# Optimization experiments

Hardware: AMD Instinct MI355X
Metric: run time of the kernel (lower is better)

Reference implementation:

```python
import jax, jax.numpy as jnp
import numpy as np

D_MODEL = 512


def _xavier(key, shape, gain=1.0):
    fan_in, fan_out = shape[1], shape[0]
    a = gain * np.sqrt(6.0 / (fan_in + fan_out))
    return jax.random.uniform(key, shape, jnp.float32, -a, a)


def setup_inputs() -> dict:
    key = jax.random.key(0)
    kx, kq, kk, kv, ko = jax.random.split(key, 5)
    x = jax.random.normal(kx, (16, D_MODEL, 32, 32), jnp.float32)
    Wq = _xavier(kq, (D_MODEL, D_MODEL))
    Wk = _xavier(kk, (D_MODEL, D_MODEL))
    Wv = _xavier(kv, (D_MODEL, D_MODEL))
    Wo = _xavier(ko, (D_MODEL, D_MODEL), gain=1e-05)
    bq = jnp.zeros((D_MODEL,), jnp.float32)
    bk = jnp.zeros((D_MODEL,), jnp.float32)
    bv = jnp.zeros((D_MODEL,), jnp.float32)
    bo = jnp.zeros((D_MODEL,), jnp.float32)
    return {"x": x, "Wq": Wq, "bq": bq, "Wk": Wk, "bk": bk, "Wv": Wv, "bv": bv, "Wo": Wo, "bo": bo}


def _proj_tokens(x, W, b):
    # 1x1 conv == channel matmul, then flatten spatial to tokens: [B, H*W, C]
    B, C, H, Wd = x.shape
    y = jnp.einsum('bchw,oc->bhwo', x, W) + b  # [B, H, W, C_out]
    return y.reshape(B, H * Wd, -1)


def reference(x, Wq, bq, Wk, bk, Wv, bv, Wo, bo):
    B, C, H, W = x.shape
    temperature = jnp.asarray(C, x.dtype) ** 0.5
    q = _proj_tokens(x, Wq, bq)  # [B, N, C]
    k = _proj_tokens(x, Wk, bk)
    v = _proj_tokens(x, Wv, bv)
    scores = jnp.einsum('bnc,bmc->bnm', q / temperature, k)  # [B, N, N]
    attention = jax.nn.softmax(scores, axis=-1)
    out = jnp.einsum('bnm,bmc->bnc', attention, v)  # [B, N, C]
    out = out.reshape(B, H, W, C)
    out = jnp.einsum('bhwc,oc->bohw', out, Wo) + bo[None, :, None, None]
    return (x + out, attention)
```

## Files before the change

### kernel.cpp

```cpp
#include <hip/hip_runtime.h>
#include <hip/hip_bf16.h>

#define DM 512
#define NTOK 1024
#define NB 16

typedef _Float16 f16;
typedef _Float16 half8 __attribute__((ext_vector_type(8)));
typedef _Float16 half4_t __attribute__((ext_vector_type(4)));
typedef float f32x4 __attribute__((ext_vector_type(4)));

__device__ __forceinline__ void gload16(const void* g, void* l) {
    __builtin_amdgcn_global_load_lds(
        (const __attribute__((address_space(1))) void*)g,
        (__attribute__((address_space(3))) void*)l, 16, 0, 0);
}

__global__ __launch_bounds__(256)
void transpose_x_kernel(const float* __restrict__ x, f16* __restrict__ xt) {
    __shared__ float tile[32][33];
    int b = blockIdx.z;
    int n0 = blockIdx.x * 32, c0 = blockIdx.y * 32;
    int tx = threadIdx.x, ty = threadIdx.y;
    const float* xb = x + (size_t)b * DM * NTOK + (size_t)(c0 + ty) * NTOK + n0 + tx * 4;
    float4 v = *(const float4*)xb;
    tile[ty][tx * 4 + 0] = v.x; tile[ty][tx * 4 + 1] = v.y;
    tile[ty][tx * 4 + 2] = v.z; tile[ty][tx * 4 + 3] = v.w;
    __syncthreads();
    half4_t h = {(f16)tile[tx * 4 + 0][ty], (f16)tile[tx * 4 + 1][ty],
                 (f16)tile[tx * 4 + 2][ty], (f16)tile[tx * 4 + 3][ty]};
    *(half4_t*)&xt[(size_t)b * NTOK * DM + (size_t)(n0 + ty) * DM + c0 + tx * 4] = h;
}

__global__ __launch_bounds__(256)
void convert_wqkv_kernel(const float* __restrict__ Wq, const float* __restrict__ Wk,
                         const float* __restrict__ Wv, const float* __restrict__ bq,
                         const float* __restrict__ bk, const float* __restrict__ bv,
                         f16* __restrict__ dst, float* __restrict__ bdst,
                         float* __restrict__ rowsum) {
    int i = blockIdx.x * 256 + threadIdx.x;
    int row = i >> 9, col = i & 511;
    float v = (row < 512) ? Wq[i] : (row < 1024) ? Wk[(row - 512) * 512 + col]
                                                 : Wv[(row - 1024) * 512 + col];
    dst[i] = (f16)v;
    if (i < 1536)
        bdst[i] = (i < 512) ? bq[i] : (i < 1024) ? bk[i - 512] : bv[i - 1024];
    if (blockIdx.x < 64) rowsum[blockIdx.x * 256 + threadIdx.x] = 0.f;
}

__global__ __launch_bounds__(256)
void convert_w_kernel(const float* __restrict__ src, f16* __restrict__ dst, int n) {
    int i = blockIdx.x * 256 + threadIdx.x;
    if (i < n) dst[i] = (f16)src[i];
}

__global__ __launch_bounds__(256)
void transpose_v_kernel(const f16* __restrict__ vtok, f16* __restrict__ vh) {
    __shared__ f16 tile[32][36];
    int b = blockIdx.z;
    int n0 = blockIdx.x * 32, c0 = blockIdx.y * 32;
    int tx = threadIdx.x, ty = threadIdx.y;
    const f16* src = vtok + (size_t)b * NTOK * DM + (size_t)(n0 + ty) * DM + c0 + tx * 4;
    half4_t v = *(const half4_t*)src;
    tile[ty][tx * 4 + 0] = v[0]; tile[ty][tx * 4 + 1] = v[1];
    tile[ty][tx * 4 + 2] = v[2]; tile[ty][tx * 4 + 3] = v[3];
    __syncthreads();
    half4_t h = {tile[tx * 4 + 0][ty], tile[tx * 4 + 1][ty],
                 tile[tx * 4 + 2][ty], tile[tx * 4 + 3][ty]};
    *(half4_t*)&vh[(size_t)b * DM * NTOK + (size_t)(c0 + ty) * NTOK + n0 + tx * 4] = h;
}

template<int MODE, int KC>
__global__ __launch_bounds__(256)
void gemm_nt(const f16* __restrict__ A, const f16* __restrict__ B, void* __restrict__ Cout,
             const float* __restrict__ bias, const float* __restrict__ resid,
             f16* __restrict__ aux, float* __restrict__ rowsum,
             int ldA, int ldB, int ldC,
             long sA, long sB, long sC, long sR, float scale) {
    __shared__ f16 As[128 * 64];
    __shared__ f16 Bs[128 * 64];
    int z = blockIdx.z;
    const f16* Ab = A + (size_t)z * sA;
    const f16* Bb = B + (size_t)z * sB;
    int tid = threadIdx.x;
    int wave = tid >> 6, lane = tid & 63;
    int wr = wave >> 1, wc = wave & 1;
    int tI = blockIdx.y * 128, tJ = blockIdx.x * 128;

    f32x4 acc[4][4];
#pragma unroll
    for (int m = 0; m < 4; ++m)
#pragma unroll
        for (int n = 0; n < 4; ++n) acc[m][n] = (f32x4){0.f, 0.f, 0.f, 0.f};

    int frow = lane & 15, fks = lane >> 4;

    for (int k0 = 0; k0 < KC; k0 += 64) {
#pragma unroll
        for (int h = 0; h < 4; ++h) {
            int L = h * 256 + tid;
            int r = L >> 3;
            int gc = ((L & 7) ^ (r & 7)) * 8;
            gload16(Ab + (size_t)(tI + r) * ldA + k0 + gc, &As[L * 8]);
            gload16(Bb + (size_t)(tJ + r) * ldB + k0 + gc, &Bs[L * 8]);
        }
        asm volatile("s_waitcnt vmcnt(0)" ::: "memory");
        __syncthreads();

#pragma unroll
        for (int ks = 0; ks < 2; ++ks) {
            half8 af[4], bf[4];
            int s = ks * 4 + fks;
#pragma unroll
            for (int m = 0; m < 4; ++m) {
                int R = wr * 64 + m * 16 + frow;
                af[m] = *(const half8*)&As[R * 64 + ((s ^ (R & 7)) << 3)];
            }
#pragma unroll
            for (int n = 0; n < 4; ++n) {
                int R = wc * 64 + n * 16 + frow;
                bf[n] = *(const half8*)&Bs[R * 64 + ((s ^ (R & 7)) << 3)];
            }
#pragma unroll
            for (int m = 0; m < 4; ++m)
#pragma unroll
                for (int n = 0; n < 4; ++n)
                    acc[m][n] = __builtin_amdgcn_mfma_f32_16x16x32_f16(af[m], bf[n], acc[m][n], 0, 0, 0);
        }
        __syncthreads();
    }

    int ro = (lane >> 4) * 4, co = lane & 15;
#pragma unroll
    for (int m = 0; m < 4; ++m) {
#pragma unroll
        for (int r = 0; r < 4; ++r) {
            int gi = tI + wr * 64 + m * 16 + ro + r;
            float rs = 0.f, inv = 0.f;
            if (MODE == 5) inv = 1.0f / rowsum[z * 1024 + gi];
#pragma unroll
            for (int n = 0; n < 4; ++n) {
                int gj = tJ + wc * 64 + n * 16 + co;
                float v = acc[m][n][r];
                if (MODE == 0) {
                    v += bias[gj];
                    if (gj < 1024)
                        ((f16*)Cout)[(size_t)z * sC + (size_t)gi * ldC + gj] = (f16)v;
                    else
                        aux[(size_t)z * 524288 + (size_t)gi * 512 + (gj - 1024)] = (f16)v;
                } else if (MODE == 2) {
                    float e = __expf(fminf(v * scale, 14.f) - 4.f);
                    ((f16*)Cout)[((size_t)z * 1024 + gi) * 2048 + 1024 + gj] = (f16)e;
                    rs += e;
                } else if (MODE == 3) {
                    ((float*)Cout)[(size_t)z * sC + (size_t)gi * ldC + gj] =
                        v + bias[gi] + resid[(size_t)z * sR + (size_t)gi * ldC + gj];
                } else {
                    ((f16*)Cout)[(size_t)z * sC + (size_t)gi * ldC + gj] = (f16)(v * inv);
                }
            }
            if (MODE == 2) {
                rs += __shfl_xor(rs, 1, 16);
                rs += __shfl_xor(rs, 2, 16);
                rs += __shfl_xor(rs, 4, 16);
                rs += __shfl_xor(rs, 8, 16);
                if ((lane & 15) == 0) atomicAdd(&rowsum[z * 1024 + gi], rs);
            }
        }
    }
}

__global__ __launch_bounds__(256)
void finalize_attn(float* __restrict__ attn, const float* __restrict__ rowsum) {
    size_t row = blockIdx.x;
    float inv = 1.0f / rowsum[row];
    float* prow = attn + row * 1024;
    half4_t h = *(const half4_t*)((const f16*)prow + 1024 + threadIdx.x * 4);
    __syncthreads();
    float4 o = {(float)h[0] * inv, (float)h[1] * inv, (float)h[2] * inv, (float)h[3] * inv};
    ((float4*)prow)[threadIdx.x] = o;
}

extern "C" void kernel_launch(void* const* d_in, const int* in_sizes, int n_in,
                              void* d_out, int out_size, void* d_ws, size_t ws_size,
                              hipStream_t stream) {
    const float* x  = (const float*)d_in[0];
    const float* Wq = (const float*)d_in[1];
    const float* bq = (const float*)d_in[2];
    const float* Wk = (const float*)d_in[3];
    const float* bk = (const float*)d_in[4];
    const float* Wv = (const float*)d_in[5];
    const float* bv = (const float*)d_in[6];
    const float* Wo = (const float*)d_in[7];
    const float* bo = (const float*)d_in[8];

    float* out0 = (float*)d_out;
    float* attn = (float*)d_out + (size_t)NB * DM * NTOK;

    f16* ws    = (f16*)d_ws;
    f16* xt    = ws;
    f16* oh    = ws;
    f16* qk    = ws + 8388608;
    f16* vh    = ws + 25165824;
    f16* wqkvh = ws + 33554432;
    f16* woh   = ws + 33554432;
    float* bqkv   = (float*)(ws + 34340864);
    float* rowsum = (float*)(ws + 34343936);

    f16* vtok = (f16*)out0;

    const long sTok   = (long)NTOK * DM;
    const long sQK    = (long)NTOK * 1024;
    const long sEslot = (long)NTOK * 2048;
    const float scal = 0.044194173824159216f;

    transpose_x_kernel<<<dim3(32, 16, NB), dim3(8, 32), 0, stream>>>(x, xt);
    convert_wqkv_kernel<<<3072, 256, 0, stream>>>(Wq, Wk, Wv, bq, bk, bv, wqkvh, bqkv, rowsum);

    gemm_nt<0, 512><<<dim3(12, 8, NB), 256, 0, stream>>>(xt, wqkvh, qk, bqkv, nullptr,
        vtok, nullptr, 512, 512, 1024, sTok, 0, sQK, 0, 0.f);

    convert_w_kernel<<<1024, 256, 0, stream>>>(Wo, woh, 262144);
    transpose_v_kernel<<<dim3(32, 16, NB), dim3(8, 32), 0, stream>>>(vtok, vh);

    gemm_nt<2, 512><<<dim3(8, 8, NB), 256, 0, stream>>>(qk, qk + 512, attn, nullptr, nullptr,
        nullptr, rowsum, 1024, 1024, 0, sQK, sQK, 0, 0, scal);

    gemm_nt<5, 1024><<<dim3(4, 8, NB), 256, 0, stream>>>((const f16*)attn + 1024, vh, oh,
        nullptr, nullptr, nullptr, rowsum, 2048, 1024, 512, sEslot, sTok, sTok, 0, 0.f);

    finalize_attn<<<NB * NTOK, 256, 0, stream>>>(attn, rowsum);

    gemm_nt<3, 512><<<dim3(8, 4, NB), 256, 0, stream>>>(woh, oh, out0, bo, x,
        nullptr, nullptr, 512, 512, 1024, 0, sTok, sTok, sTok, 0.f);
}
```

Baseline: 171.7 us.

## Merge prep kernels, fold attention finalize into output GEMM, remap workgroups

Merges the x-transpose and QKV weight conversion into one launch, and the Wo conversion and V transpose into another. The attention-normalization pass now runs as extra workgroups appended to the final output-projection GEMM, so it shares that launch instead of using its own. GEMM grids are flattened to 1D with an XCD-aware remap (flat&7 striding), so that neighbouring tiles of the same batch land on the same chiplet for L2 reuse. This cuts kernel launches and gaps between them, at the cost of divergent block roles inside each kernel and a larger finalize tile per block.

```diff
diff --git a/kernel.cpp b/kernel.cpp
--- a/kernel.cpp
+++ b/kernel.cpp
@@ -17,75 +17,105 @@
 }
 
 __global__ __launch_bounds__(256)
-void transpose_x_kernel(const float* __restrict__ x, f16* __restrict__ xt) {
+void prep_kernel(const float* __restrict__ x, f16* __restrict__ xt,
+                 const float* __restrict__ Wq, const float* __restrict__ Wk,
+                 const float* __restrict__ Wv, const float* __restrict__ bq,
+                 const float* __restrict__ bk, const float* __restrict__ bv,
+                 f16* __restrict__ wdst, float* __restrict__ bdst,
+                 float* __restrict__ rowsum) {
     __shared__ float tile[32][33];
-    int b = blockIdx.z;
-    int n0 = blockIdx.x * 32, c0 = blockIdx.y * 32;
-    int tx = threadIdx.x, ty = threadIdx.y;
-    const float* xb = x + (size_t)b * DM * NTOK + (size_t)(c0 + ty) * NTOK + n0 + tx * 4;
-    float4 v = *(const float4*)xb;
-    tile[ty][tx * 4 + 0] = v.x; tile[ty][tx * 4 + 1] = v.y;
-    tile[ty][tx * 4 + 2] = v.z; tile[ty][tx * 4 + 3] = v.w;
-    __syncthreads();
-    half4_t h = {(f16)tile[tx * 4 + 0][ty], (f16)tile[tx * 4 + 1][ty],
-                 (f16)tile[tx * 4 + 2][ty], (f16)tile[tx * 4 + 3][ty]};
-    *(half4_t*)&xt[(size_t)b * NTOK * DM + (size_t)(n0 + ty) * DM + c0 + tx * 4] = h;
+    int bid = blockIdx.x, tid = threadIdx.x;
+    if (bid < 8192) {
+        int b = bid >> 9, byy = (bid >> 5) & 15, bxx = bid & 31;
+        int n0 = bxx * 32, c0 = byy * 32;
+        int tx = tid & 7, ty = tid >> 3;
+        const float* xb = x + (size_t)b * DM * NTOK + (size_t)(c0 + ty) * NTOK + n0 + tx * 4;
+        float4 v = *(const float4*)xb;
+        tile[ty][tx * 4 + 0] = v.x; tile[ty][tx * 4 + 1] = v.y;
+        tile[ty][tx * 4 + 2] = v.z; tile[ty][tx * 4 + 3] = v.w;
+        __syncthreads();
+        half4_t h = {(f16)tile[tx * 4 + 0][ty], (f16)tile[tx * 4 + 1][ty],
+                     (f16)tile[tx * 4 + 2][ty], (f16)tile[tx * 4 + 3][ty]};
+        *(half4_t*)&xt[(size_t)b * NTOK * DM + (size_t)(n0 + ty) * DM + c0 + tx * 4] = h;
+    } else {
+        int c = bid - 8192;
+        int i = c * 256 + tid;
+        int row = i >> 9, col = i & 511;
+        float v = (row < 512) ? Wq[i] : (row < 1024) ? Wk[(row - 512) * 512 + col]
+                                                     : Wv[(row - 1024) * 512 + col];
+        wdst[i] = (f16)v;
+        if (i < 1536)
+            bdst[i] = (i < 512) ? bq[i] : (i < 1024) ? bk[i - 512] : bv[i - 1024];
+        if (c < 64) rowsum[c * 256 + tid] = 0.f;
+    }
 }
 
 __global__ __launch_bounds__(256)
-void convert_wqkv_kernel(const float* __restrict__ Wq, const float* __restrict__ Wk,
-                         const float* __restrict__ Wv, const float* __restrict__ bq,
-                         const float* __restrict__ bk, const float* __restrict__ bv,
-                         f16* __restrict__ dst, float* __restrict__ bdst,
-                         float* __restrict__ rowsum) {
-    int i = blockIdx.x * 256 + threadIdx.x;
-    int row = i >> 9, col = i & 511;
-    float v = (row < 512) ? Wq[i] : (row < 1024) ? Wk[(row - 512) * 512 + col]
-                                                 : Wv[(row - 1024) * 512 + col];
-    dst[i] = (f16)v;
-    if (i < 1536)
-        bdst[i] = (i < 512) ? bq[i] : (i < 1024) ? bk[i - 512] : bv[i - 1024];
-    if (blockIdx.x < 64) rowsum[blockIdx.x * 256 + threadIdx.x] = 0.f;
-}
-
-__global__ __launch_bounds__(256)
-void convert_w_kernel(const float* __restrict__ src, f16* __restrict__ dst, int n) {
-    int i = blockIdx.x * 256 + threadIdx.x;
-    if (i < n) dst[i] = (f16)src[i];
-}
-
-__global__ __launch_bounds__(256)
-void transpose_v_kernel(const f16* __restrict__ vtok, f16* __restrict__ vh) {
+void mid_kernel(const float* __restrict__ Wo, f16* __restrict__ woh,
+                const f16* __restrict__ vtok, f16* __restrict__ vh) {
     __shared__ f16 tile[32][36];
-    int b = blockIdx.z;
-    int n0 = blockIdx.x * 32, c0 = blockIdx.y * 32;
-    int tx = threadIdx.x, ty = threadIdx.y;
-    const f16* src = vtok + (size_t)b * NTOK * DM + (size_t)(n0 + ty) * DM + c0 + tx * 4;
-    half4_t v = *(const half4_t*)src;
-    tile[ty][tx * 4 + 0] = v[0]; tile[ty][tx * 4 + 1] = v[1];
-    tile[ty][tx * 4 + 2] = v[2]; tile[ty][tx * 4 + 3] = v[3];
-    __syncthreads();
-    half4_t h = {tile[tx * 4 + 0][ty], tile[tx * 4 + 1][ty],
-                 tile[tx * 4 + 2][ty], tile[tx * 4 + 3][ty]};
-    *(half4_t*)&vh[(size_t)b * DM * NTOK + (size_t)(c0 + ty) * NTOK + n0 + tx * 4] = h;
-}
-
-template<int MODE, int KC>
+    int bid = blockIdx.x, tid = threadIdx.x;
+    if (bid < 1024) {
+        int i = bid * 256 + tid;
+        woh[i] = (f16)Wo[i];
+    } else {
+        int c = bid - 1024;
+        int b = c >> 9, byy = (c >> 5) & 15, bxx = c & 31;
+        int n0 = bxx * 32, c0 = byy * 32;
+        int tx = tid & 7, ty = tid >> 3;
+        const f16* src = vtok + (size_t)b * NTOK * DM + (size_t)(n0 + ty) * DM + c0 + tx * 4;
+        half4_t v = *(const half4_t*)src;
+        tile[ty][tx * 4 + 0] = v[0]; tile[ty][tx * 4 + 1] = v[1];
+        tile[ty][tx * 4 + 2] = v[2]; tile[ty][tx * 4 + 3] = v[3];
+        __syncthreads();
+        half4_t h = {tile[tx * 4 + 0][ty], tile[tx * 4 + 1][ty],
+                     tile[tx * 4 + 2][ty], tile[tx * 4 + 3][ty]};
+        *(half4_t*)&vh[(size_t)b * DM * NTOK + (size_t)(c0 + ty) * NTOK + n0 + tx * 4] = h;
+    }
+}
+
+template<int MODE, int KC, int GX, int GY, int XB>
 __global__ __launch_bounds__(256)
 void gemm_nt(const f16* __restrict__ A, const f16* __restrict__ B, void* __restrict__ Cout,
              const float* __restrict__ bias, const float* __restrict__ resid,
-             f16* __restrict__ aux, float* __restrict__ rowsum,
+             f16* __restrict__ aux, float* __restrict__ rowsum, float* __restrict__ fin,
              int ldA, int ldB, int ldC,
              long sA, long sB, long sC, long sR, float scale) {
     __shared__ f16 As[128 * 64];
     __shared__ f16 Bs[128 * 64];
-    int z = blockIdx.z;
+
+    constexpr int NWG = GX * GY * NB;
+    int flat = blockIdx.x;
+    int tid = threadIdx.x;
+
+    if (MODE == 3 && flat >= NWG) {
+        int row0 = (flat - NWG) * 8;
+        const f16* eb = (const f16*)fin;
+        half4_t h[8];
+#pragma unroll
+        for (int rr = 0; rr < 8; ++rr)
+            h[rr] = *(const half4_t*)(eb + (size_t)(row0 + rr) * 2048 + 1024 + tid * 4);
+        __syncthreads();
+#pragma unroll
+        for (int rr = 0; rr < 8; ++rr) {
+            int row = row0 + rr;
+            float inv = 1.0f / rowsum[row];
+            float4 o = {(float)h[rr][0] * inv, (float)h[rr][1] * inv,
+                        (float)h[rr][2] * inv, (float)h[rr][3] * inv};
+            *(float4*)(fin + (size_t)row * 1024 + tid * 4) = o;
+        }
+        return;
+    }
+
+    int w = (flat & 7) * (NWG >> 3) + (flat >> 3);
+    int bx = w % GX, by = (w / GX) % GY, bz = w / (GX * GY);
+
+    int z = bz;
     const f16* Ab = A + (size_t)z * sA;
     const f16* Bb = B + (size_t)z * sB;
-    int tid = threadIdx.x;
     int wave = tid >> 6, lane = tid & 63;
     int wr = wave >> 1, wc = wave & 1;
-    int tI = blockIdx.y * 128, tJ = blockIdx.x * 128;
+    int tI = by * 128, tJ = bx * 128;
 
     f32x4 acc[4][4];
 #pragma unroll
@@ -170,17 +200,6 @@
     }
 }
 
-__global__ __launch_bounds__(256)
-void finalize_attn(float* __restrict__ attn, const float* __restrict__ rowsum) {
-    size_t row = blockIdx.x;
-    float inv = 1.0f / rowsum[row];
-    float* prow = attn + row * 1024;
-    half4_t h = *(const half4_t*)((const f16*)prow + 1024 + threadIdx.x * 4);
-    __syncthreads();
-    float4 o = {(float)h[0] * inv, (float)h[1] * inv, (float)h[2] * inv, (float)h[3] * inv};
-    ((float4*)prow)[threadIdx.x] = o;
-}
-
 extern "C" void kernel_launch(void* const* d_in, const int* in_sizes, int n_in,
                               void* d_out, int out_size, void* d_ws, size_t ws_size,
                               hipStream_t stream) {
@@ -214,23 +233,20 @@
     const long sEslot = (long)NTOK * 2048;
     const float scal = 0.044194173824159216f;
 
-    transpose_x_kernel<<<dim3(32, 16, NB), dim3(8, 32), 0, stream>>>(x, xt);
-    convert_wqkv_kernel<<<3072, 256, 0, stream>>>(Wq, Wk, Wv, bq, bk, bv, wqkvh, bqkv, rowsum);
-
-    gemm_nt<0, 512><<<dim3(12, 8, NB), 256, 0, stream>>>(xt, wqkvh, qk, bqkv, nullptr,
-        vtok, nullptr, 512, 512, 1024, sTok, 0, sQK, 0, 0.f);
-
-    convert_w_kernel<<<1024, 256, 0, stream>>>(Wo, woh, 262144);
-    transpose_v_kernel<<<dim3(32, 16, NB), dim3(8, 32), 0, stream>>>(vtok, vh);
-
-    gemm_nt<2, 512><<<dim3(8, 8, NB), 256, 0, stream>>>(qk, qk + 512, attn, nullptr, nullptr,
-        nullptr, rowsum, 1024, 1024, 0, sQK, sQK, 0, 0, scal);
-
-    gemm_nt<5, 1024><<<dim3(4, 8, NB), 256, 0, stream>>>((const f16*)attn + 1024, vh, oh,
-        nullptr, nullptr, nullptr, rowsum, 2048, 1024, 512, sEslot, sTok, sTok, 0, 0.f);
-
-    finalize_attn<<<NB * NTOK, 256, 0, stream>>>(attn, rowsum);
-
-    gemm_nt<3, 512><<<dim3(8, 4, NB), 256, 0, stream>>>(woh, oh, out0, bo, x,
-        nullptr, nullptr, 512, 512, 1024, 0, sTok, sTok, sTok, 0.f);
-}
+    prep_kernel<<<8192 + 3072, 256, 0, stream>>>(x, xt, Wq, Wk, Wv, bq, bk, bv,
+                                                 wqkvh, bqkv, rowsum);
+
+    gemm_nt<0, 512, 12, 8, 0><<<12 * 8 * NB, 256, 0, stream>>>(xt, wqkvh, qk, bqkv, nullptr,
+        vtok, nullptr, nullptr, 512, 512, 1024, sTok, 0, sQK, 0, 0.f);
+
+    mid_kernel<<<1024 + 8192, 256, 0, stream>>>(Wo, woh, vtok, vh);
+
+    gemm_nt<2, 512, 8, 8, 0><<<8 * 8 * NB, 256, 0, stream>>>(qk, qk + 512, attn, nullptr, nullptr,
+        nullptr, rowsum, nullptr, 1024, 1024, 0, sQK, sQK, 0, 0, scal);
+
+    gemm_nt<5, 1024, 4, 8, 0><<<4 * 8 * NB, 256, 0, stream>>>((const f16*)attn + 1024, vh, oh,
+        nullptr, nullptr, nullptr, rowsum, nullptr, 2048, 1024, 512, sEslot, sTok, sTok, 0, 0.f);
+
+    gemm_nt<3, 512, 8, 4, 2048><<<8 * 4 * NB + 2048, 256, 0, stream>>>(woh, oh, out0, bo, x,
+        nullptr, rowsum, attn, 512, 512, 1024, 0, sTok, sTok, sTok, 0.f);
+}
```

New measurement: 154.3 us. -10.1%, faster.
